# Kernel optimization log

Hardware: AMD Instinct MI355X
Metric: run time of the kernel (lower is better)

## Reference

```python
import jax, jax.numpy as jnp
import numpy as np

LEVELS = 2
_H0 = jnp.array([0.0322231, -0.01260397, -0.09921954, 0.2978578,
                 0.80373875, 0.49761867, -0.02963553, -0.07576571], dtype=jnp.float32)
_H1 = _H0[::-1] * jnp.array([-1.0, 1.0] * 4, dtype=jnp.float32)  # db4 QMF


def subband_conv2d(x, kernel_2d, stride):
    # depthwise grouped conv: same 2D kernel applied to every channel
    C = x.shape[-1]
    k = jnp.tile(kernel_2d[:, :, None, None], (1, 1, 1, C))  # HWIO with I=1, groups=C
    return jax.lax.conv_general_dilated(
        x, k, window_strides=(stride, stride), padding='SAME',
        dimension_numbers=('NHWC', 'HWIO', 'NHWC'), feature_group_count=C)


def _upsample2d(t):
    B, H, W, C = t.shape
    return jnp.zeros((B, 2 * H, 2 * W, C), t.dtype).at[:, ::2, ::2, :].set(t)


def _local_conv(t, w):
    # per-spatial-position linear map over channels: [B,H,W,I] x [I,O,W,H] -> [B,H,W,O]
    return jnp.einsum('bhwi,iowh->bhwo', t, w)


def setup_inputs() -> dict:
    key = jax.random.key(0)
    ks = jax.random.split(key, 9)
    B, H, W, C, O = 16, 128, 128, 64, 64
    inp = {
        'x': jax.random.normal(ks[0], (B, H, W, C), dtype=jnp.float32),
        'wLL': 0.02 * jax.random.normal(ks[1], (C, O, 32, 32), dtype=jnp.float32),
        'wLH_l0': 0.02 * jax.random.normal(ks[2], (C, O, 64, 64), dtype=jnp.float32),
        'wHL_l0': 0.02 * jax.random.normal(ks[3], (C, O, 64, 64), dtype=jnp.float32),
        'wHH_l0': 0.02 * jax.random.normal(ks[4], (C, O, 64, 64), dtype=jnp.float32),
        'wLH_l1': 0.02 * jax.random.normal(ks[5], (C, O, 32, 32), dtype=jnp.float32),
        'wHL_l1': 0.02 * jax.random.normal(ks[6], (C, O, 32, 32), dtype=jnp.float32),
        'wHH_l1': 0.02 * jax.random.normal(ks[7], (C, O, 32, 32), dtype=jnp.float32),
    }
    return inp


def reference(x, wLL, wLH_l0, wHL_l0, wHH_l0, wLH_l1, wHL_l1, wHH_l1):
    h0, h1 = _H0, _H1
    g0, g1 = h0[::-1], h1[::-1]
    # H=W=128 is divisible by 2**levels, so no symmetric padding is needed.
    res = x
    details = []
    for _ in range(LEVELS):
        cLL = subband_conv2d(res, jnp.outer(h0, h0), 2)
        cLH = subband_conv2d(res, jnp.outer(h0, h1), 2)
        cHL = subband_conv2d(res, jnp.outer(h1, h0), 2)
        cHH = subband_conv2d(res, jnp.outer(h1, h1), 2)
        details.append((cLH, cHL, cHH))
        res = cLL
    yA = _local_conv(res, wLL)  # [B,32,32,O]
    det_w = [(wLH_l0, wHL_l0, wHH_l0), (wLH_l1, wHL_l1, wHH_l1)]
    td = []
    for i in range(LEVELS):
        lh, hl, hh = details[i]
        wlh, whl, whh = det_w[i]
        td.append((_local_conv(lh, wlh), _local_conv(hl, whl), _local_conv(hh, whh)))
    r = yA
    for i in reversed(range(LEVELS)):
        yLH, yHL, yHH = td[i]
        r = (subband_conv2d(_upsample2d(r), jnp.outer(g0, g0), 1)
             + subband_conv2d(_upsample2d(yLH), jnp.outer(g0, g1), 1)
             + subband_conv2d(_upsample2d(yHL), jnp.outer(g1, g0), 1)
             + subband_conv2d(_upsample2d(yHH), jnp.outer(g1, g1), 1))
    return r
```

## Files before the change

### kernel.cpp

```cpp
#include <hip/hip_runtime.h>

__device__ __constant__ float H0[8] = { 0.0322231f, -0.01260397f, -0.09921954f,  0.2978578f,
                                        0.80373875f, 0.49761867f, -0.02963553f, -0.07576571f};
__device__ __constant__ float H1[8] = { 0.07576571f, -0.02963553f, -0.49761867f, 0.80373875f,
                                       -0.2978578f, -0.09921954f,  0.01260397f,  0.0322231f};
__device__ __constant__ float G0[8] = {-0.07576571f, -0.02963553f,  0.49761867f, 0.80373875f,
                                        0.2978578f,  -0.09921954f, -0.01260397f, 0.0322231f};
__device__ __constant__ float G1[8] = { 0.0322231f,   0.01260397f, -0.09921954f, -0.2978578f,
                                        0.80373875f, -0.49761867f, -0.02963553f, 0.07576571f};

template<int HIN>
__global__ __launch_bounds__(256) void fwd_dwt(const float* __restrict__ in,
                                               float* __restrict__ oLL, float* __restrict__ oLH,
                                               float* __restrict__ oHL, float* __restrict__ oHH)
{
    constexpr int OH = HIN / 2;
    constexpr int TQ = OH / 2;
    const int tid = threadIdx.x;
    const int c = tid & 63;
    const int s = blockIdx.x * 4 + (tid >> 6);
    const int j = s % TQ;
    const int i = (s / TQ) % TQ;
    const int b = s / (TQ * TQ);

    float acc[2][2][4];
#pragma unroll
    for (int a = 0; a < 2; ++a)
#pragma unroll
        for (int d = 0; d < 2; ++d)
#pragma unroll
            for (int k = 0; k < 4; ++k) acc[a][d][k] = 0.f;

    const int iw0 = 4 * j - 3;
#pragma unroll
    for (int r = 0; r < 10; ++r) {
        const int ih = 4 * i + r - 3;
        if ((unsigned)ih < (unsigned)HIN) {
            const float* row = in + ((b * HIN + ih) * HIN) * 64 + c;
            float xv[10];
#pragma unroll
            for (int v = 0; v < 10; ++v) {
                const int iw = iw0 + v;
                xv[v] = ((unsigned)iw < (unsigned)HIN) ? row[iw * 64] : 0.f;
            }
            float h00 = 0.f, h01 = 0.f, h10 = 0.f, h11 = 0.f;
#pragma unroll
            for (int v = 0; v < 8; ++v) {
                h00 += H0[v] * xv[v];
                h10 += H1[v] * xv[v];
                h01 += H0[v] * xv[v + 2];
                h11 += H1[v] * xv[v + 2];
            }
#pragma unroll
            for (int ii = 0; ii < 2; ++ii) {
                const int u = r - 2 * ii;
                if (0 <= u && u < 8) {
                    const float a0 = H0[u], a1 = H1[u];
                    acc[ii][0][0] += a0 * h00;
                    acc[ii][0][1] += a0 * h10;
                    acc[ii][0][2] += a1 * h00;
                    acc[ii][0][3] += a1 * h10;
                    acc[ii][1][0] += a0 * h01;
                    acc[ii][1][1] += a0 * h11;
                    acc[ii][1][2] += a1 * h01;
                    acc[ii][1][3] += a1 * h11;
                }
            }
        }
    }

#pragma unroll
    for (int ii = 0; ii < 2; ++ii)
#pragma unroll
        for (int jj = 0; jj < 2; ++jj) {
            const int oh = 2 * i + ii, ow = 2 * j + jj;
            const int oidx = ((b * OH + oh) * OH + ow) * 64 + c;
            oLL[oidx] = acc[ii][jj][0];
            oLH[oidx] = acc[ii][jj][1];
            oHL[oidx] = acc[ii][jj][2];
            oHH[oidx] = acc[ii][jj][3];
        }
}

template<int HD, int BJ>
__global__ __launch_bounds__(256) void local_conv(
    const float* __restrict__ t0, const float* __restrict__ t1,
    const float* __restrict__ t2, const float* __restrict__ t3,
    const float* __restrict__ w0, const float* __restrict__ w1,
    const float* __restrict__ w2, const float* __restrict__ w3,
    float* __restrict__ o0, float* __restrict__ o1,
    float* __restrict__ o2, float* __restrict__ o3)
{
    const int z = blockIdx.z;
    const float* tin = (z == 0) ? t0 : (z == 1) ? t1 : (z == 2) ? t2 : t3;
    const float* wgt = (z == 0) ? w0 : (z == 1) ? w1 : (z == 2) ? w2 : w3;
    float*       out = (z == 0) ? o0 : (z == 1) ? o1 : (z == 2) ? o2 : o3;

    const int w   = blockIdx.x;
    const int og  = blockIdx.y;
    const int tid = threadIdx.x;
    const int h   = tid % HD;
    const int bg  = tid / HD;
    constexpr int WH = HD * HD;

    float acc[BJ][16];
#pragma unroll
    for (int j = 0; j < BJ; ++j)
#pragma unroll
        for (int oo = 0; oo < 16; ++oo) acc[j][oo] = 0.f;

    for (int i4 = 0; i4 < 16; ++i4) {
        float4 tv[BJ];
#pragma unroll
        for (int j = 0; j < BJ; ++j) {
            const int b = bg * BJ + j;
            tv[j] = *(const float4*)(tin + ((b * HD + h) * HD + w) * 64 + i4 * 4);
        }
#pragma unroll
        for (int di = 0; di < 4; ++di) {
            const int i = i4 * 4 + di;
            const float* wp = wgt + (i * 64 + og * 16) * WH + w * HD + h;
#pragma unroll
            for (int oo = 0; oo < 16; ++oo) {
                const float wv = wp[oo * WH];
#pragma unroll
                for (int j = 0; j < BJ; ++j) {
                    const float tj = ((const float*)&tv[j])[di];
                    acc[j][oo] += tj * wv;
                }
            }
        }
    }

#pragma unroll
    for (int j = 0; j < BJ; ++j) {
        const int b = bg * BJ + j;
        float* op = out + ((b * HD + h) * HD + w) * 64 + og * 16;
#pragma unroll
        for (int o4 = 0; o4 < 4; ++o4) {
            float4 v = make_float4(acc[j][o4 * 4 + 0], acc[j][o4 * 4 + 1],
                                   acc[j][o4 * 4 + 2], acc[j][o4 * 4 + 3]);
            *(float4*)(op + o4 * 4) = v;
        }
    }
}

template<int HOUT>
__global__ __launch_bounds__(256) void inv_dwt(const float* __restrict__ yLL,
                                               const float* __restrict__ yLH,
                                               const float* __restrict__ yHL,
                                               const float* __restrict__ yHH,
                                               float* __restrict__ out)
{
    constexpr int HS = HOUT / 2;
    const int tid = threadIdx.x;
    const int c = tid & 63;
    const int s = blockIdx.x * 4 + (tid >> 6);
    const int j = s % HS;
    const int i = (s / HS) % HS;
    const int b = s / (HS * HS);

    float Pe[4] = {0.f, 0.f, 0.f, 0.f}, Po[4] = {0.f, 0.f, 0.f, 0.f};
    float Qe[4] = {0.f, 0.f, 0.f, 0.f}, Qo[4] = {0.f, 0.f, 0.f, 0.f};

#pragma unroll
    for (int ku = 0; ku < 4; ++ku) {
        const int m = i - 1 + ku;
        if ((unsigned)m < (unsigned)HS) {
            const float a0e = G0[1 + 2 * ku], a0o = G0[2 * ku];
            const float a1e = G1[1 + 2 * ku], a1o = G1[2 * ku];
            const int rowoff = (b * HS + m) * HS;
#pragma unroll
            for (int kv = 0; kv < 4; ++kv) {
                const int n = j - 1 + kv;
                if ((unsigned)n < (unsigned)HS) {
                    const int idx = (rowoff + n) * 64 + c;
                    const float yll = yLL[idx], ylh = yLH[idx];
                    const float yhl = yHL[idx], yhh = yHH[idx];
                    Pe[kv] += a0e * yll + a1e * yhl;
                    Po[kv] += a0o * yll + a1o * yhl;
                    Qe[kv] += a0e * ylh + a1e * yhh;
                    Qo[kv] += a0o * ylh + a1o * yhh;
                }
            }
        }
    }

    float o00 = 0.f, o01 = 0.f, o10 = 0.f, o11 = 0.f;
#pragma unroll
    for (int kv = 0; kv < 4; ++kv) {
        const float b0e = G0[1 + 2 * kv], b0o = G0[2 * kv];
        const float b1e = G1[1 + 2 * kv], b1o = G1[2 * kv];
        o00 += b0e * Pe[kv] + b1e * Qe[kv];
        o01 += b0o * Pe[kv] + b1o * Qe[kv];
        o10 += b0e * Po[kv] + b1e * Qo[kv];
        o11 += b0o * Po[kv] + b1o * Qo[kv];
    }

    const int h0 = 2 * i, w0 = 2 * j;
    const int base = ((b * HOUT + h0) * HOUT + w0) * 64 + c;
    out[base] = o00;
    out[base + 64] = o01;
    out[base + HOUT * 64] = o10;
    out[base + HOUT * 64 + 64] = o11;
}

extern "C" void kernel_launch(void* const* d_in, const int* in_sizes, int n_in,
                              void* d_out, int out_size, void* d_ws, size_t ws_size,
                              hipStream_t stream)
{
    const float* x    = (const float*)d_in[0];
    const float* wLL  = (const float*)d_in[1];
    const float* wLH0 = (const float*)d_in[2];
    const float* wHL0 = (const float*)d_in[3];
    const float* wHH0 = (const float*)d_in[4];
    const float* wLH1 = (const float*)d_in[5];
    const float* wHL1 = (const float*)d_in[6];
    const float* wHH1 = (const float*)d_in[7];
    float* out = (float*)d_out;
    float* ws  = (float*)d_ws;

    const int S0 = 16 * 64 * 64 * 64;
    const int S1 = 16 * 32 * 32 * 64;

    float* c0LL = out;
    float* c0LH = out + 1 * S0;
    float* c0HL = out + 2 * S0;
    float* c0HH = out + 3 * S0;

    float* c1   = ws;
    float* t0   = ws + 4 * S1;
    float* t1   = ws + 4 * S1 + 3 * S0;
    float* yA   = ws + 7 * S1 + 3 * S0;
    float* r1   = ws;

    fwd_dwt<128><<<16 * 32 * 32 / 4, 256, 0, stream>>>(x, c0LL, c0LH, c0HL, c0HH);

    fwd_dwt<64><<<16 * 16 * 16 / 4, 256, 0, stream>>>(c0LL,
        c1 + 0 * S1, c1 + 1 * S1, c1 + 2 * S1, c1 + 3 * S1);

    local_conv<64, 4><<<dim3(64, 4, 3), 256, 0, stream>>>(
        c0LH, c0HL, c0HH, nullptr,
        wLH0, wHL0, wHH0, nullptr,
        t0 + 0 * S0, t0 + 1 * S0, t0 + 2 * S0, nullptr);

    local_conv<32, 2><<<dim3(32, 4, 4), 256, 0, stream>>>(
        c1 + 1 * S1, c1 + 2 * S1, c1 + 3 * S1, c1 + 0 * S1,
        wLH1, wHL1, wHH1, wLL,
        t1 + 0 * S1, t1 + 1 * S1, t1 + 2 * S1, yA);

    inv_dwt<64><<<16 * 32 * 32 / 4, 256, 0, stream>>>(
        yA, t1 + 0 * S1, t1 + 1 * S1, t1 + 2 * S1, r1);

    inv_dwt<128><<<16 * 64 * 64 / 4, 256, 0, stream>>>(
        r1, t0 + 0 * S0, t0 + 1 * S0, t0 + 2 * S0, out);
}
```

Baseline: 335.2 us.

## Tile local_conv through LDS with register-blocked outer products and prefetch

Rewrites the per-position channel-mixing kernel so each block stages a 4-input-channel slice of weights (64 outputs by 16 rows) and activations (16 batches by 16 rows) into shared memory, transposed for float4 reads. Each thread then computes a 16-batch by 4-output register tile as outer products. The next chunk's global loads are issued before the compute so they overlap it. The aim is more FLOPs per loaded byte and coalesced float4 weight loads in place of strided scalar loads, at the cost of two barriers per chunk and higher register use.

```diff
diff --git a/kernel.cpp b/kernel.cpp
--- a/kernel.cpp
+++ b/kernel.cpp
@@ -82,8 +82,8 @@
         }
 }
 
-template<int HD, int BJ>
-__global__ __launch_bounds__(256) void local_conv(
+template<int HD>
+__global__ __launch_bounds__(256) void local_conv_lds(
     const float* __restrict__ t0, const float* __restrict__ t1,
     const float* __restrict__ t2, const float* __restrict__ t3,
     const float* __restrict__ w0, const float* __restrict__ w1,
@@ -91,58 +91,89 @@
     float* __restrict__ o0, float* __restrict__ o1,
     float* __restrict__ o2, float* __restrict__ o3)
 {
+    constexpr int WH  = HD * HD;
+    constexpr int HT  = 16;
+    constexpr int RSW = 76;
+    constexpr int RSA = 20;
+
+    __shared__ __align__(16) float Wl[4][HT][RSW];
+    __shared__ __align__(16) float Al[4][HT][RSA];
+
     const int z = blockIdx.z;
     const float* tin = (z == 0) ? t0 : (z == 1) ? t1 : (z == 2) ? t2 : t3;
     const float* wgt = (z == 0) ? w0 : (z == 1) ? w1 : (z == 2) ? w2 : w3;
     float*       out = (z == 0) ? o0 : (z == 1) ? o1 : (z == 2) ? o2 : o3;
 
-    const int w   = blockIdx.x;
-    const int og  = blockIdx.y;
-    const int tid = threadIdx.x;
-    const int h   = tid % HD;
-    const int bg  = tid / HD;
-    constexpr int WH = HD * HD;
-
-    float acc[BJ][16];
-#pragma unroll
-    for (int j = 0; j < BJ; ++j)
-#pragma unroll
-        for (int oo = 0; oo < 16; ++oo) acc[j][oo] = 0.f;
-
-    for (int i4 = 0; i4 < 16; ++i4) {
-        float4 tv[BJ];
-#pragma unroll
-        for (int j = 0; j < BJ; ++j) {
-            const int b = bg * BJ + j;
-            tv[j] = *(const float4*)(tin + ((b * HD + h) * HD + w) * 64 + i4 * 4);
-        }
-#pragma unroll
-        for (int di = 0; di < 4; ++di) {
-            const int i = i4 * 4 + di;
-            const float* wp = wgt + (i * 64 + og * 16) * WH + w * HD + h;
-#pragma unroll
-            for (int oo = 0; oo < 16; ++oo) {
-                const float wv = wp[oo * WH];
-#pragma unroll
-                for (int j = 0; j < BJ; ++j) {
-                    const float tj = ((const float*)&tv[j])[di];
-                    acc[j][oo] += tj * wv;
+    const int hbase = blockIdx.x * HT;
+    const int w     = blockIdx.y;
+    const int tid   = threadIdx.x;
+
+    const int so  = tid >> 2;
+    const int sh4 = tid & 3;
+    const int sb  = tid >> 4;
+    const int sha = tid & 15;
+
+    const int hc = tid & 15;
+    const int o4 = tid >> 4;
+
+    const float* wp0 = wgt + (so * WH) + w * HD + hbase + sh4 * 4;
+    const float* ap0 = tin + ((sb * HD + hbase + sha) * HD + w) * 64;
+
+    float4 acc[16];
+#pragma unroll
+    for (int b = 0; b < 16; ++b) acc[b] = make_float4(0.f, 0.f, 0.f, 0.f);
+
+    float4 wv[4], av;
+#pragma unroll
+    for (int r = 0; r < 4; ++r)
+        wv[r] = *(const float4*)(wp0 + (size_t)(r * 64) * WH);
+    av = *(const float4*)(ap0);
+
+    for (int chunk = 0; chunk < 16; ++chunk) {
+        __syncthreads();
+#pragma unroll
+        for (int r = 0; r < 4; ++r) {
+            Wl[r][sh4 * 4 + 0][so] = wv[r].x;
+            Wl[r][sh4 * 4 + 1][so] = wv[r].y;
+            Wl[r][sh4 * 4 + 2][so] = wv[r].z;
+            Wl[r][sh4 * 4 + 3][so] = wv[r].w;
+        }
+        Al[0][sha][sb] = av.x;
+        Al[1][sha][sb] = av.y;
+        Al[2][sha][sb] = av.z;
+        Al[3][sha][sb] = av.w;
+        __syncthreads();
+
+        if (chunk < 15) {
+            const int i0n = (chunk + 1) * 4;
+#pragma unroll
+            for (int r = 0; r < 4; ++r)
+                wv[r] = *(const float4*)(wp0 + (size_t)((i0n + r) * 64) * WH);
+            av = *(const float4*)(ap0 + i0n);
+        }
+
+#pragma unroll
+        for (int ii = 0; ii < 4; ++ii) {
+            const float4 wf = *(const float4*)&Wl[ii][hc][o4 * 4];
+#pragma unroll
+            for (int bq = 0; bq < 4; ++bq) {
+                const float4 af = *(const float4*)&Al[ii][hc][bq * 4];
+                const float* afp = (const float*)&af;
+#pragma unroll
+                for (int k = 0; k < 4; ++k) {
+                    const float a = afp[k];
+                    acc[bq * 4 + k].x += a * wf.x;
+                    acc[bq * 4 + k].y += a * wf.y;
+                    acc[bq * 4 + k].z += a * wf.z;
+                    acc[bq * 4 + k].w += a * wf.w;
                 }
             }
         }
     }
 
 #pragma unroll
-    for (int j = 0; j < BJ; ++j) {
-        const int b = bg * BJ + j;
-        float* op = out + ((b * HD + h) * HD + w) * 64 + og * 16;
-#pragma unroll
-        for (int o4 = 0; o4 < 4; ++o4) {
-            float4 v = make_float4(acc[j][o4 * 4 + 0], acc[j][o4 * 4 + 1],
-                                   acc[j][o4 * 4 + 2], acc[j][o4 * 4 + 3]);
-            *(float4*)(op + o4 * 4) = v;
-        }
-    }
+    for (int b = 0; b < 16; ++b)
+        *(float4*)(out + ((b * HD + hbase + hc) * HD + w) * 64 + o4 * 4) = acc[b];
 }
 
 template<int HOUT>
@@ -239,12 +270,12 @@
     fwd_dwt<64><<<16 * 16 * 16 / 4, 256, 0, stream>>>(c0LL,
         c1 + 0 * S1, c1 + 1 * S1, c1 + 2 * S1, c1 + 3 * S1);
 
-    local_conv<64, 4><<<dim3(64, 4, 3), 256, 0, stream>>>(
+    local_conv_lds<64><<<dim3(4, 64, 3), 256, 0, stream>>>(
         c0LH, c0HL, c0HH, nullptr,
         wLH0, wHL0, wHH0, nullptr,
         t0 + 0 * S0, t0 + 1 * S0, t0 + 2 * S0, nullptr);
 
-    local_conv<32, 2><<<dim3(32, 4, 4), 256, 0, stream>>>(
+    local_conv_lds<32><<<dim3(2, 32, 4), 256, 0, stream>>>(
         c1 + 1 * S1, c1 + 2 * S1, c1 + 3 * S1, c1 + 0 * S1,
         wLH1, wHL1, wHH1, wLL,
         t1 + 0 * S1, t1 + 1 * S1, t1 + 2 * S1, yA);
```

Result: faster. 291.1 us (-13.2%).
